# Performance work log

Measured on AMD Instinct MI355X. Metric: run time of the kernel, lower is better.

Reference implementation:

```python
import jax, jax.numpy as jnp
import numpy as np

CHEBY_K = 3

def _normalize_adj(A):
    # A: [B, N, N]
    A = jnp.maximum(A, 0.0)
    N = A.shape[-1]
    A = A + jnp.eye(N, dtype=A.dtype)[None, :, :]
    D = jnp.maximum(A.sum(-1), 1e-6)          # [B, N]
    D_inv_sqrt = D ** -0.5
    return D_inv_sqrt[..., :, None] * A * D_inv_sqrt[..., None, :]


def setup_inputs() -> dict:
    key = jax.random.key(0)
    k1, k2, k3, k4, k5 = jax.random.split(key, 5)
    B, N, F_in, F_out, E = 16, 512, 64, 64, 16
    x = jax.random.normal(k1, (B, N, F_in), dtype=jnp.float32)
    emb = jax.random.normal(k2, (B, N, E), dtype=jnp.float32)
    A = jax.random.uniform(k3, (B, N, N), dtype=jnp.float32)
    # xavier-uniform-like init for pools
    lim_w = float(np.sqrt(6.0 / (E * CHEBY_K * F_in + F_out)))
    weights_pool = jax.random.uniform(k4, (E, CHEBY_K, F_in, F_out), dtype=jnp.float32,
                                      minval=-lim_w, maxval=lim_w)
    lim_b = float(np.sqrt(6.0 / (E + F_out)))
    bias_pool = jax.random.uniform(k5, (E, F_out), dtype=jnp.float32,
                                   minval=-lim_b, maxval=lim_b)
    return {"x": x, "emb": emb, "A": A,
            "weights_pool": weights_pool, "bias_pool": bias_pool}


def reference(x, emb, A, weights_pool, bias_pool):
    B, N, F_in = x.shape
    K = CHEBY_K
    A_hat = _normalize_adj(A)                                   # [B,N,N]
    t0 = jnp.broadcast_to(jnp.eye(N, dtype=x.dtype)[None], (B, N, N))
    supports = [t0, A_hat]
    for _ in range(2, K):
        supports.append(2.0 * jnp.matmul(A_hat, supports[-1]) - supports[-2])
    supports = jnp.stack(supports, axis=1)                      # [B,K,N,N]
    x_g = jnp.einsum('bknm,bmf->bknf', supports, x)             # [B,K,N,F_in]
    # fused per-node adaptive conv: avoids materializing [B,K,N,F_in,F_out]
    out = jnp.einsum('bknf,bne,ekfo->bno', x_g, emb, weights_pool)
    out = out + jnp.einsum('bne,eo->bno', emb, bias_pool)       # [B,N,F_out]
    return out
```

## Files before the change

kernel.cpp:

```cpp
#include <hip/hip_runtime.h>
#include <hip/hip_bf16.h>

#define NB 16
#define NN 512
#define NF 64
#define NE 16
#define NKF 192
#define NNODE (NB*NN)

typedef __hip_bfloat16 bf16;
typedef __attribute__((ext_vector_type(8))) short short8;
typedef __attribute__((ext_vector_type(4))) float f32x4;

typedef const __attribute__((address_space(1))) char gchar;
typedef __attribute__((address_space(3))) char lchar;

__device__ inline void gload16(const void* g, void* l) {
    __builtin_amdgcn_global_load_lds((gchar*)g, (lchar*)l, 16, 0, 0);
}

__device__ inline short f2bs(float f) {
    union { bf16 b; short s; } u; u.b = __float2bfloat16(f); return u.s;
}

__global__ __launch_bounds__(256) void k_pre(
    const float* __restrict__ A, const float* __restrict__ x,
    const float* __restrict__ Wp, float* __restrict__ dis,
    bf16* __restrict__ xg, bf16* __restrict__ xT, bf16* __restrict__ Bt) {
    __shared__ float Ts[64][66];
    int bid = blockIdx.x, tid = threadIdx.x;
    if (bid < 2048) {
        int row = bid * 4 + (tid >> 6);
        int lane = tid & 63;
        const float* a = A + (size_t)row * NN;
        float s = 0.f;
        #pragma unroll
        for (int j = 0; j < NN / 64; ++j) s += fmaxf(a[lane + 64 * j], 0.f);
        #pragma unroll
        for (int off = 32; off >= 1; off >>= 1) s += __shfl_down(s, off, 64);
        if (lane == 0) dis[row] = rsqrtf(fmaxf(s + 1.0f, 1e-6f));
    } else if (bid < 2176) {
        int node0 = (bid - 2048) * 64;
        int r = tid >> 2, f0 = (tid & 3) * 16;
        const float* xp = x + (size_t)(node0 + r) * NF + f0;
        float v[16];
        #pragma unroll
        for (int i = 0; i < 16; ++i) v[i] = xp[i];
        short8 p0, p1;
        #pragma unroll
        for (int i = 0; i < 8; ++i) { p0[i] = f2bs(v[i]); p1[i] = f2bs(v[8 + i]); }
        *(short8*)&xg[(size_t)(node0 + r) * NKF + f0] = p0;
        *(short8*)&xg[(size_t)(node0 + r) * NKF + f0 + 8] = p1;
        #pragma unroll
        for (int i = 0; i < 4; ++i)
            *(float4*)&Ts[r][f0 + i * 4] = *(const float4*)(v + i * 4);
        __syncthreads();
        int f = tid >> 2, nq0 = (tid & 3) * 16;
        int b = node0 >> 9, nloc = node0 & (NN - 1);
        bf16* xt = xT + (size_t)(b * NF + f) * NN + nloc + nq0;
        #pragma unroll
        for (int h = 0; h < 2; ++h) {
            short8 o;
            #pragma unroll
            for (int i = 0; i < 8; ++i) o[i] = f2bs(Ts[nq0 + h * 8 + i][f]);
            *(short8*)&xt[h * 8] = o;
        }
    } else {
        int q = bid - 2176;
        int e = q / 3, kt = q % 3;
        int r = tid >> 2, o0 = (tid & 3) * 16;
        const float* wp = Wp + (size_t)e * (NKF * NF) + (size_t)(kt * 64 + r) * NF + o0;
        #pragma unroll
        for (int i = 0; i < 4; ++i)
            *(float4*)&Ts[r][o0 + i * 4] = *(const float4*)(wp + i * 4);
        __syncthreads();
        int o = tid >> 2, r0 = (tid & 3) * 16;
        bf16* bt = Bt + (size_t)(e * 64 + o) * NKF + kt * 64 + r0;
        #pragma unroll
        for (int h = 0; h < 2; ++h) {
            short8 w;
            #pragma unroll
            for (int i = 0; i < 8; ++i) w[i] = f2bs(Ts[r0 + h * 8 + i][o]);
            *(short8*)&bt[h * 8] = w;
        }
    }
}

__global__ __launch_bounds__(256) void k_ahat(
    const float* __restrict__ A, const float* __restrict__ dis,
    bf16* __restrict__ Ah) {
    int tid = threadIdx.x;
    int row = blockIdx.x * 4 + (tid >> 6);
    int m0 = (tid & 63) * 8;
    int b = row >> 9, n = row & (NN - 1);
    const float* db = dis + b * NN;
    float dn = db[n];
    const float* ap = A + (size_t)row * NN + m0;
    float4 a0 = *(const float4*)ap, a1 = *(const float4*)(ap + 4);
    float4 d0 = *(const float4*)(db + m0), d1 = *(const float4*)(db + m0 + 4);
    float av[8] = {a0.x, a0.y, a0.z, a0.w, a1.x, a1.y, a1.z, a1.w};
    float dm[8] = {d0.x, d0.y, d0.z, d0.w, d1.x, d1.y, d1.z, d1.w};
    short8 o;
    #pragma unroll
    for (int i = 0; i < 8; ++i) {
        float v = fmaxf(av[i], 0.f) + ((n == m0 + i) ? 1.f : 0.f);
        o[i] = f2bs(v * dn * dm[i]);
    }
    *(short8*)&Ah[(size_t)row * NN + m0] = o;
}

template <int PASS>
__global__ __launch_bounds__(256) void k_spmm(
    const short* __restrict__ Ah, const short* __restrict__ Bsrc,
    const float* __restrict__ x, bf16* __restrict__ xg, bf16* __restrict__ y1T) {
    __shared__ short As[64 * 32];
    __shared__ short Xs[64 * 32];
    __shared__ float Cs[64][66];
    int tid = threadIdx.x, lane = tid & 63, w = tid >> 6;
    int n0 = blockIdx.x * 64, b = blockIdx.y;
    const short* Ab = Ah + (size_t)b * NN * NN;
    const short* Xb = Bsrc + (size_t)b * NF * NN;

    int sr = tid >> 2;
    int p  = tid & 3;
    int cA = p ^ ((sr >> 1) & 3);

    int fr = lane & 15;
    int fc = ((lane >> 4) ^ ((fr >> 1) & 3)) * 8;

    f32x4 acc[4] = {};

    for (int kt = 0; kt < 16; ++kt) {
        __syncthreads();
        gload16(Ab + (size_t)(n0 + sr) * NN + kt * 32 + cA * 8, As + tid * 8);
        gload16(Xb + (size_t)sr * NN + kt * 32 + cA * 8, Xs + tid * 8);
        __syncthreads();
        short8 afr = *(const short8*)&As[(16 * w + fr) * 32 + fc];
        #pragma unroll
        for (int j = 0; j < 4; ++j) {
            short8 bfr = *(const short8*)&Xs[(16 * j + fr) * 32 + fc];
            acc[j] = __builtin_amdgcn_mfma_f32_16x16x32_bf16(afr, bfr, acc[j], 0, 0, 0);
        }
    }

    #pragma unroll
    for (int j = 0; j < 4; ++j)
        #pragma unroll
        for (int r = 0; r < 4; ++r)
            Cs[16 * w + 4 * (lane >> 4) + r][16 * j + (lane & 15)] = acc[j][r];
    __syncthreads();

    int nl = tid >> 2, f0 = (tid & 3) * 16;
    size_t node = (size_t)b * NN + n0 + nl;
    float cv[16];
    #pragma unroll
    for (int i = 0; i < 16; ++i) cv[i] = Cs[nl][f0 + i];
    if (PASS == 0) {
        short8 p0, p1;
        #pragma unroll
        for (int i = 0; i < 8; ++i) { p0[i] = f2bs(cv[i]); p1[i] = f2bs(cv[8 + i]); }
        *(short8*)&xg[node * NKF + 64 + f0] = p0;
        *(short8*)&xg[node * NKF + 64 + f0 + 8] = p1;
        int f = tid >> 2, nq0 = (tid & 3) * 16;
        bf16* yt = y1T + (size_t)(b * NF + f) * NN + n0 + nq0;
        #pragma unroll
        for (int h = 0; h < 2; ++h) {
            short8 o;
            #pragma unroll
            for (int i = 0; i < 8; ++i) o[i] = f2bs(Cs[nq0 + h * 8 + i][f]);
            *(short8*)&yt[h * 8] = o;
        }
    } else {
        const float* xp = x + node * NF + f0;
        short8 p0, p1;
        #pragma unroll
        for (int i = 0; i < 8; ++i) {
            p0[i] = f2bs(2.f * cv[i] - xp[i]);
            p1[i] = f2bs(2.f * cv[8 + i] - xp[8 + i]);
        }
        *(short8*)&xg[node * NKF + 128 + f0] = p0;
        *(short8*)&xg[node * NKF + 128 + f0 + 8] = p1;
    }
}

__global__ __launch_bounds__(256) void k_gemm(
    const short* __restrict__ xg, const short* __restrict__ Bt,
    bf16* __restrict__ t) {
    __shared__ short As[128 * 32];
    __shared__ short Bs[128 * 32];
    int tid = threadIdx.x;
    int lane = tid & 63;
    int w = tid >> 6;
    int n0 = blockIdx.x * 128;
    int c0 = blockIdx.y * 128;

    int rA0 = tid >> 2;
    int p   = tid & 3;
    int cA  = p ^ ((rA0 >> 1) & 3);

    int fr = lane & 15;
    int fc = ((lane >> 4) ^ ((fr >> 1) & 3)) * 8;

    f32x4 acc[4][4] = {};

    for (int kt = 0; kt < 6; ++kt) {
        __syncthreads();
        gload16(xg + (size_t)(n0 + rA0) * NKF + kt * 32 + cA * 8, As + tid * 8);
        gload16(xg + (size_t)(n0 + rA0 + 64) * NKF + kt * 32 + cA * 8, As + 2048 + tid * 8);
        gload16(Bt + (size_t)(c0 + rA0) * NKF + kt * 32 + cA * 8, Bs + tid * 8);
        gload16(Bt + (size_t)(c0 + rA0 + 64) * NKF + kt * 32 + cA * 8, Bs + 2048 + tid * 8);
        __syncthreads();

        int wr = w >> 1, wc = w & 1;
        short8 a[4], bfr[4];
        #pragma unroll
        for (int i = 0; i < 4; ++i)
            a[i] = *(const short8*)&As[(wr * 64 + i * 16 + fr) * 32 + fc];
        #pragma unroll
        for (int j = 0; j < 4; ++j)
            bfr[j] = *(const short8*)&Bs[(wc * 64 + j * 16 + fr) * 32 + fc];
        #pragma unroll
        for (int i = 0; i < 4; ++i)
            #pragma unroll
            for (int j = 0; j < 4; ++j)
                acc[i][j] = __builtin_amdgcn_mfma_f32_16x16x32_bf16(a[i], bfr[j], acc[i][j], 0, 0, 0);
    }

    int wr = w >> 1, wc = w & 1;
    #pragma unroll
    for (int i = 0; i < 4; ++i) {
        #pragma unroll
        for (int j = 0; j < 4; ++j) {
            #pragma unroll
            for (int r = 0; r < 4; ++r) {
                int m = n0 + wr * 64 + i * 16 + (lane >> 4) * 4 + r;
                int cc = c0 + wc * 64 + j * 16 + (lane & 15);
                t[(size_t)m * 1024 + cc] = __float2bfloat16(acc[i][j][r]);
            }
        }
    }
}

__global__ void k_reduce(const bf16* __restrict__ t, const float* __restrict__ emb,
                         const float* __restrict__ bp, float* __restrict__ out) {
    int gid = blockIdx.x * 256 + threadIdx.x;
    int node = gid >> 6, o = gid & 63;
    float s = 0.f;
    #pragma unroll
    for (int e = 0; e < NE; ++e) {
        float tv = __bfloat162float(t[(size_t)node * 1024 + e * 64 + o]);
        s = fmaf(emb[(size_t)node * NE + e], tv + bp[e * 64 + o], s);
    }
    out[gid] = s;
}

extern "C" void kernel_launch(void* const* d_in, const int* in_sizes, int n_in,
                              void* d_out, int out_size, void* d_ws, size_t ws_size,
                              hipStream_t stream) {
    const float* x   = (const float*)d_in[0];
    const float* emb = (const float*)d_in[1];
    const float* A   = (const float*)d_in[2];
    const float* Wp  = (const float*)d_in[3];
    const float* bp  = (const float*)d_in[4];
    float* out = (float*)d_out;

    float* ws  = (float*)d_ws;
    float* dis = ws;
    bf16*  xT  = (bf16*)(ws + 8192);
    bf16*  y1T = (bf16*)(ws + 270336);
    bf16*  xg  = (bf16*)(ws + 532480);
    bf16*  Bt  = (bf16*)(ws + 1318912);
    bf16*  t   = (bf16*)(ws + 1417216);
    bf16*  Ah  = (bf16*)(ws + 5611520);

    k_pre<<<2224, 256, 0, stream>>>(A, x, Wp, dis, xg, xT, Bt);
    k_ahat<<<2048, 256, 0, stream>>>(A, dis, Ah);
    dim3 g2(NN / 64, NB);
    k_spmm<0><<<g2, 256, 0, stream>>>((const short*)Ah, (const short*)xT, x, xg, y1T);
    k_spmm<1><<<g2, 256, 0, stream>>>((const short*)Ah, (const short*)y1T, x, xg, y1T);
    dim3 gg(NNODE / 128, 8);
    k_gemm<<<gg, 256, 0, stream>>>((const short*)xg, (const short*)Bt, t);
    k_reduce<<<NNODE * NF / 256, 256, 0, stream>>>(t, emb, bp, out);
}
```

Baseline: 44.26 us.

## Fuse adaptive-weight GEMM with embedding reduction to skip intermediate tensor

Merges the node-by-(E*F_out) GEMM and the embedding-weighted reduction into one kernel. Each block keeps 32 nodes' xg fragments in registers and double-buffers each embedding slice of the weight matrix in LDS, applying emb and bias straight into per-node output accumulators. This removes the write and re-read of the large bf16 intermediate t plus one launch. In exchange the grid shrinks to 256 blocks, and each block does 16 sequential e-iterations with a barrier each.

```diff
diff --git a/kernel.cpp b/kernel.cpp
--- a/kernel.cpp
+++ b/kernel.cpp
@@ -183,75 +183,86 @@
     }
 }
 
-__global__ __launch_bounds__(256) void k_gemm(
+__global__ __launch_bounds__(256) void k_fused(
     const short* __restrict__ xg, const short* __restrict__ Bt,
-    bf16* __restrict__ t) {
-    __shared__ short As[128 * 32];
-    __shared__ short Bs[128 * 32];
-    int tid = threadIdx.x;
-    int lane = tid & 63;
-    int w = tid >> 6;
-    int n0 = blockIdx.x * 128;
-    int c0 = blockIdx.y * 128;
-
-    int rA0 = tid >> 2;
-    int p   = tid & 3;
-    int cA  = p ^ ((rA0 >> 1) & 3);
-
-    int fr = lane & 15;
-    int fc = ((lane >> 4) ^ ((fr >> 1) & 3)) * 8;
-
-    f32x4 acc[4][4] = {};
-
-    for (int kt = 0; kt < 6; ++kt) {
-        __syncthreads();
-        gload16(xg + (size_t)(n0 + rA0) * NKF + kt * 32 + cA * 8, As + tid * 8);
-        gload16(xg + (size_t)(n0 + rA0 + 64) * NKF + kt * 32 + cA * 8, As + 2048 + tid * 8);
-        gload16(Bt + (size_t)(c0 + rA0) * NKF + kt * 32 + cA * 8, Bs + tid * 8);
-        gload16(Bt + (size_t)(c0 + rA0 + 64) * NKF + kt * 32 + cA * 8, Bs + 2048 + tid * 8);
-        __syncthreads();
-
-        int wr = w >> 1, wc = w & 1;
-        short8 a[4], bfr[4];
-        #pragma unroll
-        for (int i = 0; i < 4; ++i)
-            a[i] = *(const short8*)&As[(wr * 64 + i * 16 + fr) * 32 + fc];
-        #pragma unroll
-        for (int j = 0; j < 4; ++j)
-            bfr[j] = *(const short8*)&Bs[(wc * 64 + j * 16 + fr) * 32 + fc];
-        #pragma unroll
-        for (int i = 0; i < 4; ++i)
-            #pragma unroll
-            for (int j = 0; j < 4; ++j)
-                acc[i][j] = __builtin_amdgcn_mfma_f32_16x16x32_bf16(a[i], bfr[j], acc[i][j], 0, 0, 0);
-    }
-
-    int wr = w >> 1, wc = w & 1;
-    #pragma unroll
-    for (int i = 0; i < 4; ++i) {
-        #pragma unroll
-        for (int j = 0; j < 4; ++j) {
+    const float* __restrict__ emb, const float* __restrict__ bpool,
+    float* __restrict__ out) {
+    __shared__ short Axs[32 * 192];
+    __shared__ short Bts[2][64 * 192];
+    int tid = threadIdx.x, lane = tid & 63, w = tid >> 6;
+    int node0 = blockIdx.x * 32;
+
+    {
+        int kk0 = tid >> 7;
+        int r = (tid >> 2) & 31;
+        int slot = tid & 3;
+        int cA = slot ^ ((r >> 1) & 3);
+        #pragma unroll
+        for (int h = 0; h < 3; ++h) {
+            int kk = h * 2 + kk0;
+            gload16(xg + (size_t)(node0 + r) * NKF + kk * 32 + cA * 8,
+                    Axs + h * 2048 + tid * 8);
+        }
+    }
+    int br = tid >> 2, bslot = tid & 3;
+    int bcA = bslot ^ ((br >> 1) & 3);
+    #pragma unroll
+    for (int kk = 0; kk < 6; ++kk)
+        gload16(Bt + (size_t)(0 * 64 + br) * NKF + kk * 32 + bcA * 8,
+                Bts[0] + kk * 2048 + br * 32 + bslot * 8);
+    __syncthreads();
+
+    int fr = lane & 15, ak = lane >> 4;
+    int arow = 16 * (w & 1) + fr;
+    short8 afr[6];
+    #pragma unroll
+    for (int kk = 0; kk < 6; ++kk)
+        afr[kk] = *(const short8*)&Axs[kk * 1024 + arow * 32 + ((ak ^ ((arow >> 1) & 3)) * 8)];
+
+    float oacc[2][4] = {};
+    int cur = 0;
+    for (int e = 0; e < NE; ++e) {
+        if (e < NE - 1) {
+            #pragma unroll
+            for (int kk = 0; kk < 6; ++kk)
+                gload16(Bt + (size_t)((e + 1) * 64 + br) * NKF + kk * 32 + bcA * 8,
+                        Bts[cur ^ 1] + kk * 2048 + br * 32 + bslot * 8);
+        }
+        f32x4 acc[2] = {};
+        #pragma unroll
+        for (int j = 0; j < 2; ++j) {
+            int brow = 32 * (w >> 1) + 16 * j + fr;
+            #pragma unroll
+            for (int kk = 0; kk < 6; ++kk) {
+                short8 bfr = *(const short8*)&Bts[cur][kk * 2048 + brow * 32 +
+                                                       ((ak ^ ((brow >> 1) & 3)) * 8)];
+                acc[j] = __builtin_amdgcn_mfma_f32_16x16x32_bf16(afr[kk], bfr, acc[j], 0, 0, 0);
+            }
+        }
+        #pragma unroll
+        for (int j = 0; j < 2; ++j) {
+            int col = 32 * (w >> 1) + 16 * j + fr;
+            float bv = bpool[e * NF + col];
             #pragma unroll
             for (int r = 0; r < 4; ++r) {
-                int m = n0 + wr * 64 + i * 16 + (lane >> 4) * 4 + r;
-                int cc = c0 + wc * 64 + j * 16 + (lane & 15);
-                t[(size_t)m * 1024 + cc] = __float2bfloat16(acc[i][j][r]);
+                int nl = 16 * (w & 1) + ak * 4 + r;
+                float ev = emb[(size_t)(node0 + nl) * NE + e];
+                oacc[j][r] = fmaf(ev, acc[j][r] + bv, oacc[j][r]);
             }
         }
-    }
-}
-
-__global__ void k_reduce(const bf16* __restrict__ t, const float* __restrict__ emb,
-                         const float* __restrict__ bp, float* __restrict__ out) {
-    int gid = blockIdx.x * 256 + threadIdx.x;
-    int node = gid >> 6, o = gid & 63;
-    float s = 0.f;
-    #pragma unroll
-    for (int e = 0; e < NE; ++e) {
-        float tv = __bfloat162float(t[(size_t)node * 1024 + e * 64 + o]);
-        s = fmaf(emb[(size_t)node * NE + e], tv + bp[e * 64 + o], s);
-    }
-    out[gid] = s;
+        __syncthreads();
+        cur ^= 1;
+    }
+
+    #pragma unroll
+    for (int j = 0; j < 2; ++j) {
+        int col = 32 * (w >> 1) + 16 * j + fr;
+        #pragma unroll
+        for (int r = 0; r < 4; ++r) {
+            int nl = 16 * (w & 1) + ak * 4 + r;
+            out[(size_t)(node0 + nl) * NF + col] = oacc[j][r];
+        }
+    }
 }
 
 extern "C" void kernel_launch(void* const* d_in, const int* in_sizes, int n_in,
@@ -270,15 +281,12 @@
     bf16*  y1T = (bf16*)(ws + 270336);
     bf16*  xg  = (bf16*)(ws + 532480);
     bf16*  Bt  = (bf16*)(ws + 1318912);
-    bf16*  t   = (bf16*)(ws + 1417216);
-    bf16*  Ah  = (bf16*)(ws + 5611520);
+    bf16*  Ah  = (bf16*)(ws + 1417216);
 
     k_pre<<<2224, 256, 0, stream>>>(A, x, Wp, dis, xg, xT, Bt);
     k_ahat<<<2048, 256, 0, stream>>>(A, dis, Ah);
     dim3 g2(NN / 64, NB);
     k_spmm<0><<<g2, 256, 0, stream>>>((const short*)Ah, (const short*)xT, x, xg, y1T);
     k_spmm<1><<<g2, 256, 0, stream>>>((const short*)Ah, (const short*)y1T, x, xg, y1T);
-    dim3 gg(NNODE / 128, 8);
-    k_gemm<<<gg, 256, 0, stream>>>((const short*)xg, (const short*)Bt, t);
-    k_reduce<<<NNODE * NF / 256, 256, 0, stream>>>(t, emb, bp, out);
-}
+    k_fused<<<NNODE / 32, 256, 0, stream>>>((const short*)xg, (const short*)Bt, emb, bp, out);
+}
```

New measurement: 48.39 us. 9.3% more time.
